# Performance work log

Hardware: AMD Instinct MI355X
Metric: run time of the kernel (lower is better)

The kernel has to match this reference:

```python
import jax, jax.numpy as jnp
import numpy as np


def _approx_match(xyz1, xyz2):
    """Faithful port of approxmatch_cpu/cuda (auction-style soft bipartite matching).

    xyz1: [b, n, 3], xyz2: [b, m, 3] -> (match [b, n, m], sq_dists [b, n, m])
    """
    b, n, _ = xyz1.shape
    m = xyz2.shape[1]
    factorl = max(n, m) // n  # integer division, as in the CUDA source
    factorr = max(n, m) // m

    # all-pairs squared distances  [b, n, m]
    d2 = jnp.sum((xyz1[:, :, None, :] - xyz2[:, None, :, :]) ** 2, axis=-1)

    # annealing schedule: j = 8 .. -1 -> level = -4^j ; j = -2 -> level = 0
    levels = jnp.asarray([-(4.0 ** j) for j in range(8, -2, -1)] + [0.0],
                         dtype=xyz1.dtype)

    satl0 = jnp.full((b, n), float(factorl), dtype=xyz1.dtype)  # row capacities
    satr0 = jnp.full((b, m), float(factorr), dtype=xyz1.dtype)  # col capacities
    match0 = jnp.zeros((b, n, m), dtype=xyz1.dtype)

    def step(carry, level):
        satl, satr, match = carry
        # weight = exp(level * d2) * saturatedr
        w = jnp.exp(level * d2) * satr[:, None, :]                       # [b,n,m]
        # row-normalize, scale by remaining row capacity
        w = w / (jnp.sum(w, axis=2, keepdims=True) + 1e-9) * satl[:, :, None]
        # column rescale by remaining column capacity
        ss = jnp.sum(w, axis=1) + 1e-9                                   # [b,m]
        w = w * (satr / ss)[:, None, :]
        # deplete capacities
        satl = jnp.maximum(satl - jnp.sum(w, axis=2), 0.0)
        satr = jnp.maximum(satr - jnp.sum(w, axis=1), 0.0)
        return (satl, satr, match + w), None

    (_, _, match), _ = jax.lax.scan(step, (satl0, satr0, match0), levels)
    return match, d2


def setup_inputs() -> dict:
    key = jax.random.key(0)
    k1, k2 = jax.random.split(key)
    b, n, m = 4, 4096, 4096
    return {
        "input1": jax.random.normal(k1, (b, n, 3), dtype=jnp.float32),
        "input2": jax.random.normal(k2, (b, m, 3), dtype=jnp.float32),
        "eps": 0,    # accepted but unused by the original Function
        "iters": 50, # accepted but unused by the original Function
    }


def reference(input1, input2, eps, iters):
    # eps / iters are ignored, matching EarthMoverDistanceFunction.apply(xyz1, xyz2)
    match, d2 = _approx_match(input1, input2)
    dist = jnp.sqrt(jnp.maximum(d2, 1e-12))  # matchcost uses euclidean (sqrt) distance
    return jnp.sum(match * dist, axis=(1, 2))  # cost per batch element, [b]
```

## Files before the change

kernel.cpp:

```cpp
#include <hip/hip_runtime.h>

#define BLOCK 256
#define IC    64
#define RPT   4
#define ROWS  (BLOCK*RPT)
#define RBLK  64

__device__ __forceinline__ float wave_reduce_add(float v) {
#pragma unroll
    for (int off = 32; off > 0; off >>= 1) v += __shfl_down(v, off, 64);
    return v;
}
__device__ __forceinline__ float lg2(float x) { return __builtin_amdgcn_logf(x); }
__device__ __forceinline__ float ex2(float x) { return __builtin_amdgcn_exp2f(x); }

__device__ __forceinline__ void load_rows(const float* p, float* x, float* y, float* z) {
    float4 v0 = *(const float4*)p;
    float4 v1 = *(const float4*)(p + 4);
    float4 v2 = *(const float4*)(p + 8);
    x[0]=v0.x; x[1]=v0.w; x[2]=v1.z; x[3]=v2.y;
    y[0]=v0.y; y[1]=v1.x; y[2]=v1.w; y[3]=v2.z;
    z[0]=v0.z; z[1]=v1.y; z[2]=v2.x; z[3]=v2.w;
}

__global__ __launch_bounds__(BLOCK)
void emd_init(float* __restrict__ satl, float* __restrict__ satr,
              float* __restrict__ out, float* __restrict__ Asum,
              float fl, float fr, int b, int n, int m) {
    int idx = blockIdx.x * blockDim.x + threadIdx.x;
    if (idx < b * n) satl[idx] = fl;
    if (idx < b * m) satr[idx] = fr;
    if (idx < b)   { out[idx] = 0.f; Asum[idx] = 0.f; }
}

__global__ __launch_bounds__(BLOCK, 4)
void emd_pass1(const float* __restrict__ xyz1, const float* __restrict__ xyz2,
               float* __restrict__ P1p, float ls, float wconst, float thr,
               int n, int m, int bn)
{
    __shared__ float4 sh[IC];
    const int bb = blockIdx.z, chunk = blockIdx.y;

    const int i0 = blockIdx.x * ROWS + threadIdx.x * RPT;
    float x[RPT], y[RPT], z[RPT], acc[RPT];
    load_rows(xyz1 + ((size_t)bb * n + i0) * 3, x, y, z);

    const float* x2 = xyz2 + (size_t)bb * m * 3;
    for (int t = threadIdx.x; t < IC; t += BLOCK) {
        int j = chunk * IC + t;
        sh[t] = make_float4(x2[3*j], x2[3*j+1], x2[3*j+2], wconst);
    }
    __syncthreads();

#pragma unroll
    for (int r = 0; r < RPT; ++r) acc[r] = 0.f;
#pragma unroll 2
    for (int tb = 0; tb < IC; tb += 4) {
        float4 q0 = sh[tb+0], q1 = sh[tb+1], q2 = sh[tb+2], q3 = sh[tb+3];
        float d0[RPT], d1[RPT], d2v[RPT], d3[RPT];
        float dmin = 1e30f;
#pragma unroll
        for (int r = 0; r < RPT; ++r) {
            float dx, dy, dz;
            dx=x[r]-q0.x; dy=y[r]-q0.y; dz=z[r]-q0.z; d0[r]=fmaf(dz,dz,fmaf(dy,dy,dx*dx));
            dx=x[r]-q1.x; dy=y[r]-q1.y; dz=z[r]-q1.z; d1[r]=fmaf(dz,dz,fmaf(dy,dy,dx*dx));
            dx=x[r]-q2.x; dy=y[r]-q2.y; dz=z[r]-q2.z; d2v[r]=fmaf(dz,dz,fmaf(dy,dy,dx*dx));
            dx=x[r]-q3.x; dy=y[r]-q3.y; dz=z[r]-q3.z; d3[r]=fmaf(dz,dz,fmaf(dy,dy,dx*dx));
            dmin = fminf(dmin, fminf(fminf(d0[r], d1[r]), fminf(d2v[r], d3[r])));
        }
        if (__any(dmin < thr)) {
#pragma unroll
            for (int r = 0; r < RPT; ++r) {
                acc[r] += ex2(fmaf(d0[r],  ls, q0.w));
                acc[r] += ex2(fmaf(d1[r],  ls, q1.w));
                acc[r] += ex2(fmaf(d2v[r], ls, q2.w));
                acc[r] += ex2(fmaf(d3[r],  ls, q3.w));
            }
        }
    }
    *(float4*)&P1p[(size_t)chunk * bn + (size_t)bb * n + i0] =
        make_float4(acc[0], acc[1], acc[2], acc[3]);
}

__global__ __launch_bounds__(BLOCK, 4)
void emd_pass2(const float* __restrict__ xyzO, const float* __restrict__ xyzS,
               const float* __restrict__ satlIn, float* __restrict__ satlOut,
               const float* __restrict__ aIn, float* __restrict__ aOut,
               const float* __restrict__ P1p, const float* __restrict__ P3a,
               const float* __restrict__ P3b, float* __restrict__ P2p,
               float* __restrict__ cost,
               float ls, float thr, int nO, int nS, int bnS, int bnO,
               int C4, int first)
{
    __shared__ float4 sh[IC];
    __shared__ float red[3][4][IC];
    const int bb = blockIdx.z, chunk = blockIdx.y;

    const int j0 = blockIdx.x * ROWS + threadIdx.x * RPT;
    float x[RPT], y[RPT], z[RPT], acc[RPT];
    load_rows(xyzO + ((size_t)bb * nO + j0) * 3, x, y, z);

    const int t6 = threadIdx.x & 63, g = threadIdx.x >> 6;
    const size_t ri = (size_t)bb * nS + chunk * IC + t6;
    {
        float ps = 0.f, pa = 0.f, pb = 0.f;
        const int c0 = g * C4;
        if (first) {
#pragma unroll 16
            for (int k = 0; k < C4; ++k) ps += P1p[(size_t)(c0 + k) * bnS + ri];
        } else {
#pragma unroll 16
            for (int k = 0; k < C4; ++k) {
                ps += P1p[(size_t)(c0 + k) * bnS + ri];
                pa += P3a[(size_t)(c0 + k) * bnS + ri];
                pb += P3b[(size_t)(c0 + k) * bnS + ri];
            }
        }
        red[0][g][t6] = ps; red[1][g][t6] = pa; red[2][g][t6] = pb;
    }
    __syncthreads();
    if (threadIdx.x < IC) {
        float rs = red[0][0][t6] + red[0][1][t6] + red[0][2][t6] + red[0][3][t6];
        float sl, costv = 0.f;
        if (first) {
            sl = satlIn[ri];
        } else {
            float s1 = red[1][0][t6] + red[1][1][t6] + red[1][2][t6] + red[1][3][t6];
            float s2 = red[2][0][t6] + red[2][1][t6] + red[2][2][t6] + red[2][3][t6];
            float ap = aIn[ri];
            sl = fmaxf(satlIn[ri] - ap * s1, 0.f);
            costv = ap * s2;
        }
        float av = sl / (rs + 1e-9f);
        if (blockIdx.x == 0) {
            satlOut[ri] = sl;
            aOut[ri]    = av;
            if (!first) {
                float cv = wave_reduce_add(costv);
                if (t6 == 0) atomicAdd(&cost[bb], cv);
            }
        }
        const float* xs = xyzS + ((size_t)bb * nS + chunk * IC + t6) * 3;
        sh[t6] = make_float4(xs[0], xs[1], xs[2], lg2(av));
    }
    __syncthreads();

#pragma unroll
    for (int r = 0; r < RPT; ++r) acc[r] = 0.f;
    if (thr < 1e29f) {
#pragma unroll 2
        for (int tb = 0; tb < IC; tb += 4) {
            float4 q0 = sh[tb+0], q1 = sh[tb+1], q2 = sh[tb+2], q3 = sh[tb+3];
            float d0[RPT], d1[RPT], d2v[RPT], d3[RPT];
            float dmin = 1e30f;
#pragma unroll
            for (int r = 0; r < RPT; ++r) {
                float dx, dy, dz;
                dx=x[r]-q0.x; dy=y[r]-q0.y; dz=z[r]-q0.z; d0[r]=fmaf(dz,dz,fmaf(dy,dy,dx*dx));
                dx=x[r]-q1.x; dy=y[r]-q1.y; dz=z[r]-q1.z; d1[r]=fmaf(dz,dz,fmaf(dy,dy,dx*dx));
                dx=x[r]-q2.x; dy=y[r]-q2.y; dz=z[r]-q2.z; d2v[r]=fmaf(dz,dz,fmaf(dy,dy,dx*dx));
                dx=x[r]-q3.x; dy=y[r]-q3.y; dz=z[r]-q3.z; d3[r]=fmaf(dz,dz,fmaf(dy,dy,dx*dx));
                dmin = fminf(dmin, fminf(fminf(d0[r], d1[r]), fminf(d2v[r], d3[r])));
            }
            if (__any(dmin < thr)) {
#pragma unroll
                for (int r = 0; r < RPT; ++r) {
                    acc[r] += ex2(fmaf(d0[r],  ls, q0.w));
                    acc[r] += ex2(fmaf(d1[r],  ls, q1.w));
                    acc[r] += ex2(fmaf(d2v[r], ls, q2.w));
                    acc[r] += ex2(fmaf(d3[r],  ls, q3.w));
                }
            }
        }
    } else {
#pragma unroll 2
        for (int tb = 0; tb < IC; tb += 4) {
            float4 q0 = sh[tb+0], q1 = sh[tb+1], q2 = sh[tb+2], q3 = sh[tb+3];
#pragma unroll
            for (int r = 0; r < RPT; ++r) {
                float dx, dy, dz, d2;
                dx=x[r]-q0.x; dy=y[r]-q0.y; dz=z[r]-q0.z;
                d2=fmaf(dz,dz,fmaf(dy,dy,dx*dx)); acc[r] += ex2(fmaf(d2, ls, q0.w));
                dx=x[r]-q1.x; dy=y[r]-q1.y; dz=z[r]-q1.z;
                d2=fmaf(dz,dz,fmaf(dy,dy,dx*dx)); acc[r] += ex2(fmaf(d2, ls, q1.w));
                dx=x[r]-q2.x; dy=y[r]-q2.y; dz=z[r]-q2.z;
                d2=fmaf(dz,dz,fmaf(dy,dy,dx*dx)); acc[r] += ex2(fmaf(d2, ls, q2.w));
                dx=x[r]-q3.x; dy=y[r]-q3.y; dz=z[r]-q3.z;
                d2=fmaf(dz,dz,fmaf(dy,dy,dx*dx)); acc[r] += ex2(fmaf(d2, ls, q3.w));
            }
        }
    }
    *(float4*)&P2p[(size_t)chunk * bnO + (size_t)bb * nO + j0] =
        make_float4(acc[0], acc[1], acc[2], acc[3]);
}

__global__ __launch_bounds__(BLOCK, 4)
void emd_fused(const float* __restrict__ xyz1, const float* __restrict__ xyz2,
               const float* __restrict__ satrIn, float* __restrict__ satrOut,
               const float* __restrict__ P2p,
               float* __restrict__ P3a, float* __restrict__ P3b,
               float* __restrict__ P1p,
               float lsA, float lsB, float thr,
               int n, int m, int bn, int bm, int C4, int mode)
{
    __shared__ float4 sh[IC];
    __shared__ float  shB[IC];
    __shared__ float  red[4][IC];
    __shared__ float  snsumS;
    const int bb = blockIdx.z, chunk = blockIdx.y;

    const int i0 = blockIdx.x * ROWS + threadIdx.x * RPT;
    float x[RPT], y[RPT], z[RPT];
    load_rows(xyz1 + ((size_t)bb * n + i0) * 3, x, y, z);

    const int t6 = threadIdx.x & 63, g = threadIdx.x >> 6;
    const size_t rj = (size_t)bb * m + chunk * IC + t6;
    {
        float ps = 0.f;
        const int c0 = g * C4;
#pragma unroll 16
        for (int k = 0; k < C4; ++k) ps += P2p[(size_t)(c0 + k) * bm + rj];
        red[g][t6] = ps;
    }
    __syncthreads();
    if (threadIdx.x < IC) {
        float cs  = red[0][t6] + red[1][t6] + red[2][t6] + red[3][t6];
        float sr  = satrIn[rj];
        float cs2 = sr * cs;
        float inv = sr / (cs2 + 1e-9f);
        float r2  = sr * inv;
        float sn  = fmaxf(sr - cs2 * inv, 0.f);
        if (blockIdx.x == 0) satrOut[rj] = sn;
        const float* xs = xyz2 + ((size_t)bb * m + chunk * IC + t6) * 3;
        if (mode == 0) {
            sh[t6]  = make_float4(xs[0], xs[1], xs[2], lg2(r2));
            shB[t6] = lg2(sn);
        } else {
            sh[t6]  = make_float4(xs[0], xs[1], xs[2], r2);
            shB[t6] = sn;
            if (mode == 2) {
                float ss = wave_reduce_add(sn);
                if (t6 == 0) snsumS = ss;
            }
        }
    }
    __syncthreads();

    float s1[RPT], s2[RPT], r1[RPT];
#pragma unroll
    for (int r = 0; r < RPT; ++r) { s1[r] = 0.f; s2[r] = 0.f; r1[r] = 0.f; }

    if (mode == 0) {
#pragma unroll 2
        for (int tb = 0; tb < IC; tb += 4) {
            float4 q0 = sh[tb+0], q1 = sh[tb+1], q2 = sh[tb+2], q3 = sh[tb+3];
            float lb0 = shB[tb+0], lb1 = shB[tb+1], lb2 = shB[tb+2], lb3 = shB[tb+3];
            float d0[RPT], d1[RPT], d2v[RPT], d3[RPT];
            float dmin = 1e30f;
#pragma unroll
            for (int r = 0; r < RPT; ++r) {
                float dx, dy, dz;
                dx=x[r]-q0.x; dy=y[r]-q0.y; dz=z[r]-q0.z; d0[r]=fmaf(dz,dz,fmaf(dy,dy,dx*dx));
                dx=x[r]-q1.x; dy=y[r]-q1.y; dz=z[r]-q1.z; d1[r]=fmaf(dz,dz,fmaf(dy,dy,dx*dx));
                dx=x[r]-q2.x; dy=y[r]-q2.y; dz=z[r]-q2.z; d2v[r]=fmaf(dz,dz,fmaf(dy,dy,dx*dx));
                dx=x[r]-q3.x; dy=y[r]-q3.y; dz=z[r]-q3.z; d3[r]=fmaf(dz,dz,fmaf(dy,dy,dx*dx));
                dmin = fminf(dmin, fminf(fminf(d0[r], d1[r]), fminf(d2v[r], d3[r])));
            }
            if (__any(dmin < thr)) {
#pragma unroll
                for (int r = 0; r < RPT; ++r) {
                    float e;
                    e = ex2(fmaf(d0[r], lsA, q0.w));
                    s1[r] += e; s2[r] = fmaf(e, __builtin_amdgcn_sqrtf(d0[r]), s2[r]);
                    r1[r] += ex2(fmaf(d0[r], lsB, lb0));
                    e = ex2(fmaf(d1[r], lsA, q1.w));
                    s1[r] += e; s2[r] = fmaf(e, __builtin_amdgcn_sqrtf(d1[r]), s2[r]);
                    r1[r] += ex2(fmaf(d1[r], lsB, lb1));
                    e = ex2(fmaf(d2v[r], lsA, q2.w));
                    s1[r] += e; s2[r] = fmaf(e, __builtin_amdgcn_sqrtf(d2v[r]), s2[r]);
                    r1[r] += ex2(fmaf(d2v[r], lsB, lb2));
                    e = ex2(fmaf(d3[r], lsA, q3.w));
                    s1[r] += e; s2[r] = fmaf(e, __builtin_amdgcn_sqrtf(d3[r]), s2[r]);
                    r1[r] += ex2(fmaf(d3[r], lsB, lb3));
                }
            }
        }
    } else if (mode == 1) {
#pragma unroll 2
        for (int tb = 0; tb < IC; tb += 4) {
            float4 q0 = sh[tb+0], q1 = sh[tb+1], q2 = sh[tb+2], q3 = sh[tb+3];
            float lb0 = shB[tb+0], lb1 = shB[tb+1], lb2 = shB[tb+2], lb3 = shB[tb+3];
#pragma unroll
            for (int r = 0; r < RPT; ++r) {
                float dx, dy, dz, d2, t, t2, e3;
                dx=x[r]-q0.x; dy=y[r]-q0.y; dz=z[r]-q0.z;
                d2=fmaf(dz,dz,fmaf(dy,dy,dx*dx));
                t = ex2(d2 * lsB); t2 = t*t; e3 = t2*t2*q0.w;
                s1[r] += e3; s2[r] = fmaf(e3, __builtin_amdgcn_sqrtf(d2), s2[r]);
                r1[r] = fmaf(t, lb0, r1[r]);
                dx=x[r]-q1.x; dy=y[r]-q1.y; dz=z[r]-q1.z;
                d2=fmaf(dz,dz,fmaf(dy,dy,dx*dx));
                t = ex2(d2 * lsB); t2 = t*t; e3 = t2*t2*q1.w;
                s1[r] += e3; s2[r] = fmaf(e3, __builtin_amdgcn_sqrtf(d2), s2[r]);
                r1[r] = fmaf(t, lb1, r1[r]);
                dx=x[r]-q2.x; dy=y[r]-q2.y; dz=z[r]-q2.z;
                d2=fmaf(dz,dz,fmaf(dy,dy,dx*dx));
                t = ex2(d2 * lsB); t2 = t*t; e3 = t2*t2*q2.w;
                s1[r] += e3; s2[r] = fmaf(e3, __builtin_amdgcn_sqrtf(d2), s2[r]);
                r1[r] = fmaf(t, lb2, r1[r]);
                dx=x[r]-q3.x; dy=y[r]-q3.y; dz=z[r]-q3.z;
                d2=fmaf(dz,dz,fmaf(dy,dy,dx*dx));
                t = ex2(d2 * lsB); t2 = t*t; e3 = t2*t2*q3.w;
                s1[r] += e3; s2[r] = fmaf(e3, __builtin_amdgcn_sqrtf(d2), s2[r]);
                r1[r] = fmaf(t, lb3, r1[r]);
            }
        }
    } else {
#pragma unroll 2
        for (int tb = 0; tb < IC; tb += 4) {
            float4 q0 = sh[tb+0], q1 = sh[tb+1], q2 = sh[tb+2], q3 = sh[tb+3];
#pragma unroll
            for (int r = 0; r < RPT; ++r) {
                float dx, dy, dz, d2, e;
                dx=x[r]-q0.x; dy=y[r]-q0.y; dz=z[r]-q0.z;
                d2=fmaf(dz,dz,fmaf(dy,dy,dx*dx));
                e = ex2(d2 * lsA) * q0.w;
                s1[r] += e; s2[r] = fmaf(e, __builtin_amdgcn_sqrtf(d2), s2[r]);
                dx=x[r]-q1.x; dy=y[r]-q1.y; dz=z[r]-q1.z;
                d2=fmaf(dz,dz,fmaf(dy,dy,dx*dx));
                e = ex2(d2 * lsA) * q1.w;
                s1[r] += e; s2[r] = fmaf(e, __builtin_amdgcn_sqrtf(d2), s2[r]);
                dx=x[r]-q2.x; dy=y[r]-q2.y; dz=z[r]-q2.z;
                d2=fmaf(dz,dz,fmaf(dy,dy,dx*dx));
                e = ex2(d2 * lsA) * q2.w;
                s1[r] += e; s2[r] = fmaf(e, __builtin_amdgcn_sqrtf(d2), s2[r]);
                dx=x[r]-q3.x; dy=y[r]-q3.y; dz=z[r]-q3.z;
                d2=fmaf(dz,dz,fmaf(dy,dy,dx*dx));
                e = ex2(d2 * lsA) * q3.w;
                s1[r] += e; s2[r] = fmaf(e, __builtin_amdgcn_sqrtf(d2), s2[r]);
            }
        }
    }
    size_t base = (size_t)chunk * bn + (size_t)bb * n + i0;
    if (mode == 2) {
        float sc = snsumS;
#pragma unroll
        for (int r = 0; r < RPT; ++r) r1[r] = sc;
    }
    *(float4*)&P3a[base] = make_float4(s1[0], s1[1], s1[2], s1[3]);
    *(float4*)&P3b[base] = make_float4(s2[0], s2[1], s2[2], s2[3]);
    *(float4*)&P1p[base] = make_float4(r1[0], r1[1], r1[2], r1[3]);
}

__global__ __launch_bounds__(BLOCK)
void emd_redL_last(const float* __restrict__ satl, const float* __restrict__ aIn,
                   float* __restrict__ aOut,
                   const float* __restrict__ P1p, const float* __restrict__ P3a,
                   const float* __restrict__ P3b, float* __restrict__ cost,
                   float* __restrict__ Asum, int C, int bn, int n)
{
    const int idx = blockIdx.x * BLOCK + threadIdx.x;
    float rs = 0.f, s1 = 0.f, s2 = 0.f;
#pragma unroll 16
    for (int c = 0; c < C; ++c) {
        rs += P1p[(size_t)c * bn + idx];
        s1 += P3a[(size_t)c * bn + idx];
        s2 += P3b[(size_t)c * bn + idx];
    }
    float ap = aIn[idx];
    float sl = fmaxf(satl[idx] - ap * s1, 0.f);
    float av = sl / (rs + 1e-9f);
    aOut[idx] = av;
    float cv  = wave_reduce_add(ap * s2);
    float avs = wave_reduce_add(av);
    if ((threadIdx.x & 63) == 0) {
        atomicAdd(&cost[idx / n], cv);
        atomicAdd(&Asum[idx / n], avs);
    }
}

__global__ __launch_bounds__(BLOCK, 4)
void emd_pass3_last(const float* __restrict__ xyz1, const float* __restrict__ xyz2,
                    const float* __restrict__ satrIn, const float* __restrict__ Asum,
                    float* __restrict__ P3b, int n, int m, int bn, int bm)
{
    __shared__ float4 sh[IC];
    const int bb = blockIdx.z, chunk = blockIdx.y;

    const int i0 = blockIdx.x * ROWS + threadIdx.x * RPT;
    float x[RPT], y[RPT], z[RPT], s2[RPT];
    load_rows(xyz1 + ((size_t)bb * n + i0) * 3, x, y, z);

    const float A = Asum[bb];
    for (int t = threadIdx.x; t < IC; t += BLOCK) {
        int j = chunk * IC + t;
        size_t rj = (size_t)bb * m + j;
        float sr  = satrIn[rj];
        float cs2 = sr * A;
        float inv = sr / (cs2 + 1e-9f);
        const float* xs = xyz2 + ((size_t)bb * m + j) * 3;
        sh[t] = make_float4(xs[0], xs[1], xs[2], sr * inv);
    }
    __syncthreads();

#pragma unroll
    for (int r = 0; r < RPT; ++r) s2[r] = 0.f;
#pragma unroll 4
    for (int tb = 0; tb < IC; tb += 4) {
        float4 q0 = sh[tb+0], q1 = sh[tb+1], q2 = sh[tb+2], q3 = sh[tb+3];
#pragma unroll
        for (int r = 0; r < RPT; ++r) {
            float dx, dy, dz, d2;
            dx = x[r]-q0.x; dy = y[r]-q0.y; dz = z[r]-q0.z;
            d2 = fmaf(dz, dz, fmaf(dy, dy, dx*dx));
            s2[r] = fmaf(q0.w, __builtin_amdgcn_sqrtf(d2), s2[r]);
            dx = x[r]-q1.x; dy = y[r]-q1.y; dz = z[r]-q1.z;
            d2 = fmaf(dz, dz, fmaf(dy, dy, dx*dx));
            s2[r] = fmaf(q1.w, __builtin_amdgcn_sqrtf(d2), s2[r]);
            dx = x[r]-q2.x; dy = y[r]-q2.y; dz = z[r]-q2.z;
            d2 = fmaf(dz, dz, fmaf(dy, dy, dx*dx));
            s2[r] = fmaf(q2.w, __builtin_amdgcn_sqrtf(d2), s2[r]);
            dx = x[r]-q3.x; dy = y[r]-q3.y; dz = z[r]-q3.z;
            d2 = fmaf(dz, dz, fmaf(dy, dy, dx*dx));
            s2[r] = fmaf(q3.w, __builtin_amdgcn_sqrtf(d2), s2[r]);
        }
    }
    *(float4*)&P3b[(size_t)chunk * bn + (size_t)bb * n + i0] =
        make_float4(s2[0], s2[1], s2[2], s2[3]);
}

__global__ __launch_bounds__(RBLK)
void emd_final(const float* __restrict__ a, const float* __restrict__ P3b,
               float* __restrict__ cost, int C, int bn, int n)
{
    const int idx = blockIdx.x * RBLK + threadIdx.x;
    float s2 = 0.f;
#pragma unroll 16
    for (int c = 0; c < C; ++c) s2 += P3b[(size_t)c * bn + idx];
    float cv = wave_reduce_add(a[idx] * s2);
    if (threadIdx.x == 0) atomicAdd(&cost[idx / n], cv);
}

extern "C" void kernel_launch(void* const* d_in, const int* in_sizes, int n_in,
                              void* d_out, int out_size, void* d_ws, size_t ws_size,
                              hipStream_t stream)
{
    const float* xyz1 = (const float*)d_in[0];
    const float* xyz2 = (const float*)d_in[1];
    const int b = out_size;
    const int n = in_sizes[0] / (3 * b);
    const int m = in_sizes[1] / (3 * b);
    const int C  = m / IC;
    const int C2 = n / IC;
    const int bn = b * n, bm = b * m;

    float* ws    = (float*)d_ws;
    float* satlA = ws; ws += (size_t)bn;
    float* satlB = ws; ws += (size_t)bn;
    float* satrA = ws; ws += (size_t)bm;
    float* satrB = ws; ws += (size_t)bm;
    float* aA    = ws; ws += (size_t)bn;
    float* aB    = ws; ws += (size_t)bn;
    float* Asum  = ws; ws += 16;
    float* P1p   = ws; ws += (size_t)bn * C;
    float* P2p   = ws; ws += (size_t)bm * C2;
    float* P3a   = ws; ws += (size_t)bn * C;
    float* P3b   = ws; ws += (size_t)bn * C;

    float* out = (float*)d_out;

    const int mx = n > m ? n : m;
    const float fl = (float)(mx / n), fr = (float)(mx / m);
    const float lgfr = log2f(fr);

    emd_init<<<dim3((b * mx + BLOCK - 1) / BLOCK), BLOCK, 0, stream>>>(
        satlA, satrA, out, Asum, fl, fr, b, n, m);

    const double LOG2E = 1.4426950408889634074;
    const double levels[11] = {-65536.0, -16384.0, -4096.0, -1024.0, -256.0,
                               -64.0, -16.0, -4.0, -1.0, -0.25, 0.0};
    float lsv[11], thrP[11], thrF[10];
    for (int k = 0; k < 11; ++k) {
        lsv[k] = (float)(levels[k] * LOG2E);
        thrP[k] = (k <= 3) ? 165.f / fabsf(lsv[k]) : 1e30f;
    }
    for (int k = 0; k < 10; ++k)
        thrF[k] = (k <= 3) ? 165.f / fabsf(lsv[k]) : 1e30f;

    const dim3 g1(n / ROWS, m / IC, b);
    const dim3 g2(m / ROWS, n / IC, b);

    emd_pass1<<<g1, BLOCK, 0, stream>>>(xyz1, xyz2, P1p, lsv[0], lgfr, thrP[0],
                                        n, m, bn);

    float *slI = satlA, *slO = satlB, *aI = aA, *aO = aB;
    float *srI = satrA, *srO = satrB;
    for (int L = 0; L <= 9; ++L) {
        emd_pass2<<<g2, BLOCK, 0, stream>>>(xyz2, xyz1, slI, slO, aI, aO,
                                            P1p, P3a, P3b, P2p, out,
                                            lsv[L], thrP[L], m, n, bn, bm,
                                            C / 4, (L == 0) ? 1 : 0);
        { float* t = slI; slI = slO; slO = t; }
        { float* t = aI;  aI  = aO;  aO  = t; }
        const int mode = (L <= 3) ? 0 : ((L <= 8) ? 1 : 2);
        emd_fused<<<g1, BLOCK, 0, stream>>>(xyz1, xyz2, srI, srO, P2p,
                                            P3a, P3b, P1p,
                                            lsv[L], lsv[L + 1], thrF[L],
                                            n, m, bn, bm, C2 / 4, mode);
        { float* t = srI; srI = srO; srO = t; }
    }
    emd_redL_last<<<dim3(bn / BLOCK), BLOCK, 0, stream>>>(
        slI, aI, aO, P1p, P3a, P3b, out, Asum, C, bn, n);
    emd_pass3_last<<<g1, BLOCK, 0, stream>>>(xyz1, xyz2, srI, Asum, P3b,
                                             n, m, bn, bm);
    emd_final<<<dim3(bn / RBLK), RBLK, 0, stream>>>(aO, P3b, out, C, bn, n);
}
```

Measured before the change: 686.2 us.

## Halve column chunk size and double occupancy target across pairwise kernels

```diff
diff --git a/kernel.cpp b/kernel.cpp
--- a/kernel.cpp
+++ b/kernel.cpp
@@ -1,7 +1,7 @@
 #include <hip/hip_runtime.h>
 
 #define BLOCK 256
-#define IC    64
+#define IC    32
 #define RPT   4
 #define ROWS  (BLOCK*RPT)
 #define RBLK  64
@@ -33,7 +33,7 @@
     if (idx < b)   { out[idx] = 0.f; Asum[idx] = 0.f; }
 }
 
-__global__ __launch_bounds__(BLOCK, 4)
+__global__ __launch_bounds__(BLOCK, 8)
 void emd_pass1(const float* __restrict__ xyz1, const float* __restrict__ xyz2,
                float* __restrict__ P1p, float ls, float wconst, float thr,
                int n, int m, int bn)
@@ -46,9 +46,9 @@
     load_rows(xyz1 + ((size_t)bb * n + i0) * 3, x, y, z);
 
     const float* x2 = xyz2 + (size_t)bb * m * 3;
-    for (int t = threadIdx.x; t < IC; t += BLOCK) {
-        int j = chunk * IC + t;
-        sh[t] = make_float4(x2[3*j], x2[3*j+1], x2[3*j+2], wconst);
+    if (threadIdx.x < IC) {
+        int j = chunk * IC + threadIdx.x;
+        sh[threadIdx.x] = make_float4(x2[3*j], x2[3*j+1], x2[3*j+2], wconst);
     }
     __syncthreads();
 
@@ -82,7 +82,7 @@
         make_float4(acc[0], acc[1], acc[2], acc[3]);
 }
 
-__global__ __launch_bounds__(BLOCK, 4)
+__global__ __launch_bounds__(BLOCK, 8)
 void emd_pass2(const float* __restrict__ xyzO, const float* __restrict__ xyzS,
                const float* __restrict__ satlIn, float* __restrict__ satlOut,
                const float* __restrict__ aIn, float* __restrict__ aOut,
@@ -90,58 +90,66 @@
                const float* __restrict__ P3b, float* __restrict__ P2p,
                float* __restrict__ cost,
                float ls, float thr, int nO, int nS, int bnS, int bnO,
-               int C4, int first)
+               int C8, int first)
 {
     __shared__ float4 sh[IC];
-    __shared__ float red[3][4][IC];
+    __shared__ float red[3][8][IC];
     const int bb = blockIdx.z, chunk = blockIdx.y;
 
     const int j0 = blockIdx.x * ROWS + threadIdx.x * RPT;
     float x[RPT], y[RPT], z[RPT], acc[RPT];
     load_rows(xyzO + ((size_t)bb * nO + j0) * 3, x, y, z);
 
-    const int t6 = threadIdx.x & 63, g = threadIdx.x >> 6;
-    const size_t ri = (size_t)bb * nS + chunk * IC + t6;
     {
+        const int t5 = threadIdx.x & 31, g = threadIdx.x >> 5;
+        const size_t ri = (size_t)bb * nS + chunk * IC + t5;
         float ps = 0.f, pa = 0.f, pb = 0.f;
-        const int c0 = g * C4;
+        const int c0 = g * C8;
         if (first) {
 #pragma unroll 16
-            for (int k = 0; k < C4; ++k) ps += P1p[(size_t)(c0 + k) * bnS + ri];
+            for (int k = 0; k < C8; ++k) ps += P1p[(size_t)(c0 + k) * bnS + ri];
         } else {
 #pragma unroll 16
-            for (int k = 0; k < C4; ++k) {
+            for (int k = 0; k < C8; ++k) {
                 ps += P1p[(size_t)(c0 + k) * bnS + ri];
                 pa += P3a[(size_t)(c0 + k) * bnS + ri];
                 pb += P3b[(size_t)(c0 + k) * bnS + ri];
             }
         }
-        red[0][g][t6] = ps; red[1][g][t6] = pa; red[2][g][t6] = pb;
+        red[0][g][t5] = ps; red[1][g][t5] = pa; red[2][g][t5] = pb;
     }
     __syncthreads();
-    if (threadIdx.x < IC) {
-        float rs = red[0][0][t6] + red[0][1][t6] + red[0][2][t6] + red[0][3][t6];
-        float sl, costv = 0.f;
+    if (threadIdx.x < 64) {
+        const int t = threadIdx.x;
+        const bool act = t < IC;
+        const size_t ri = (size_t)bb * nS + chunk * IC + (act ? t : 0);
+        float rs = 0.f, s1 = 0.f, s2 = 0.f;
+        if (act) {
+#pragma unroll
+            for (int g = 0; g < 8; ++g) {
+                rs += red[0][g][t]; s1 += red[1][g][t]; s2 += red[2][g][t];
+            }
+        }
+        float sl = 0.f, costv = 0.f;
         if (first) {
-            sl = satlIn[ri];
+            if (act) sl = satlIn[ri];
         } else {
-            float s1 = red[1][0][t6] + red[1][1][t6] + red[1][2][t6] + red[1][3][t6];
-            float s2 = red[2][0][t6] + red[2][1][t6] + red[2][2][t6] + red[2][3][t6];
-            float ap = aIn[ri];
-            sl = fmaxf(satlIn[ri] - ap * s1, 0.f);
+            float ap = act ? aIn[ri] : 0.f;
+            if (act) sl = fmaxf(satlIn[ri] - ap * s1, 0.f);
             costv = ap * s2;
         }
-        float av = sl / (rs + 1e-9f);
+        float av = act ? sl / (rs + 1e-9f) : 0.f;
         if (blockIdx.x == 0) {
-            satlOut[ri] = sl;
-            aOut[ri]    = av;
+            if (act) { satlOut[ri] = sl; aOut[ri] = av; }
             if (!first) {
                 float cv = wave_reduce_add(costv);
-                if (t6 == 0) atomicAdd(&cost[bb], cv);
-            }
-        }
-        const float* xs = xyzS + ((size_t)bb * nS + chunk * IC + t6) * 3;
-        sh[t6] = make_float4(xs[0], xs[1], xs[2], lg2(av));
+                if (t == 0) atomicAdd(&cost[bb], cv);
+            }
+        }
+        if (act) {
+            const float* xs = xyzS + ri * 3;
+            sh[t] = make_float4(xs[0], xs[1], xs[2], lg2(av));
+        }
     }
     __syncthreads();
 
@@ -194,18 +202,18 @@
         make_float4(acc[0], acc[1], acc[2], acc[3]);
 }
 
-__global__ __launch_bounds__(BLOCK, 4)
+__global__ __launch_bounds__(BLOCK, 8)
 void emd_fused(const float* __restrict__ xyz1, const float* __restrict__ xyz2,
                const float* __restrict__ satrIn, float* __restrict__ satrOut,
                const float* __restrict__ P2p,
                float* __restrict__ P3a, float* __restrict__ P3b,
                float* __restrict__ P1p,
                float lsA, float lsB, float thr,
-               int n, int m, int bn, int bm, int C4, int mode)
+               int n, int m, int bn, int bm, int C8, int mode)
 {
     __shared__ float4 sh[IC];
     __shared__ float  shB[IC];
-    __shared__ float  red[4][IC];
+    __shared__ float  red[8][IC];
     __shared__ float  snsumS;
     const int bb = blockIdx.z, chunk = blockIdx.y;
 
@@ -213,35 +221,43 @@
     float x[RPT], y[RPT], z[RPT];
     load_rows(xyz1 + ((size_t)bb * n + i0) * 3, x, y, z);
 
-    const int t6 = threadIdx.x & 63, g = threadIdx.x >> 6;
-    const size_t rj = (size_t)bb * m + chunk * IC + t6;
     {
+        const int t5 = threadIdx.x & 31, g = threadIdx.x >> 5;
+        const size_t rj = (size_t)bb * m + chunk * IC + t5;
         float ps = 0.f;
-        const int c0 = g * C4;
+        const int c0 = g * C8;
 #pragma unroll 16
-        for (int k = 0; k < C4; ++k) ps += P2p[(size_t)(c0 + k) * bm + rj];
-        red[g][t6] = ps;
+        for (int k = 0; k < C8; ++k) ps += P2p[(size_t)(c0 + k) * bm + rj];
+        red[g][t5] = ps;
     }
     __syncthreads();
-    if (threadIdx.x < IC) {
-        float cs  = red[0][t6] + red[1][t6] + red[2][t6] + red[3][t6];
-        float sr  = satrIn[rj];
-        float cs2 = sr * cs;
-        float inv = sr / (cs2 + 1e-9f);
-        float r2  = sr * inv;
-        float sn  = fmaxf(sr - cs2 * inv, 0.f);
-        if (blockIdx.x == 0) satrOut[rj] = sn;
-        const float* xs = xyz2 + ((size_t)bb * m + chunk * IC + t6) * 3;
-        if (mode == 0) {
-            sh[t6]  = make_float4(xs[0], xs[1], xs[2], lg2(r2));
-            shB[t6] = lg2(sn);
-        } else {
-            sh[t6]  = make_float4(xs[0], xs[1], xs[2], r2);
-            shB[t6] = sn;
-            if (mode == 2) {
-                float ss = wave_reduce_add(sn);
-                if (t6 == 0) snsumS = ss;
-            }
+    if (threadIdx.x < 64) {
+        const int t = threadIdx.x;
+        const bool act = t < IC;
+        const size_t rj = (size_t)bb * m + chunk * IC + (act ? t : 0);
+        float sn = 0.f;
+        if (act) {
+            float cs = 0.f;
+#pragma unroll
+            for (int g = 0; g < 8; ++g) cs += red[g][t];
+            float sr  = satrIn[rj];
+            float cs2 = sr * cs;
+            float inv = sr / (cs2 + 1e-9f);
+            float r2  = sr * inv;
+            sn = fmaxf(sr - cs2 * inv, 0.f);
+            if (blockIdx.x == 0) satrOut[rj] = sn;
+            const float* xs = xyz2 + rj * 3;
+            if (mode == 0) {
+                sh[t]  = make_float4(xs[0], xs[1], xs[2], lg2(r2));
+                shB[t] = lg2(sn);
+            } else {
+                sh[t]  = make_float4(xs[0], xs[1], xs[2], r2);
+                shB[t] = sn;
+            }
+        }
+        if (mode == 2) {
+            float ss = wave_reduce_add(act ? sn : 0.f);
+            if (t == 0) snsumS = ss;
         }
     }
     __syncthreads();
@@ -379,7 +395,7 @@
     }
 }
 
-__global__ __launch_bounds__(BLOCK, 4)
+__global__ __launch_bounds__(BLOCK, 8)
 void emd_pass3_last(const float* __restrict__ xyz1, const float* __restrict__ xyz2,
                     const float* __restrict__ satrIn, const float* __restrict__ Asum,
                     float* __restrict__ P3b, int n, int m, int bn, int bm)
@@ -391,15 +407,15 @@
     float x[RPT], y[RPT], z[RPT], s2[RPT];
     load_rows(xyz1 + ((size_t)bb * n + i0) * 3, x, y, z);
 
-    const float A = Asum[bb];
-    for (int t = threadIdx.x; t < IC; t += BLOCK) {
-        int j = chunk * IC + t;
+    if (threadIdx.x < IC) {
+        const float A = Asum[bb];
+        int j = chunk * IC + threadIdx.x;
         size_t rj = (size_t)bb * m + j;
         float sr  = satrIn[rj];
         float cs2 = sr * A;
         float inv = sr / (cs2 + 1e-9f);
-        const float* xs = xyz2 + ((size_t)bb * m + j) * 3;
-        sh[t] = make_float4(xs[0], xs[1], xs[2], sr * inv);
+        const float* xs = xyz2 + rj * 3;
+        sh[threadIdx.x] = make_float4(xs[0], xs[1], xs[2], sr * inv);
     }
     __syncthreads();
 
@@ -499,14 +515,14 @@
         emd_pass2<<<g2, BLOCK, 0, stream>>>(xyz2, xyz1, slI, slO, aI, aO,
                                             P1p, P3a, P3b, P2p, out,
                                             lsv[L], thrP[L], m, n, bn, bm,
-                                            C / 4, (L == 0) ? 1 : 0);
+                                            C / 8, (L == 0) ? 1 : 0);
         { float* t = slI; slI = slO; slO = t; }
         { float* t = aI;  aI  = aO;  aO  = t; }
         const int mode = (L <= 3) ? 0 : ((L <= 8) ? 1 : 2);
         emd_fused<<<g1, BLOCK, 0, stream>>>(xyz1, xyz2, srI, srO, P2p,
                                             P3a, P3b, P1p,
                                             lsv[L], lsv[L + 1], thrF[L],
-                                            n, m, bn, bm, C2 / 4, mode);
+                                            n, m, bn, bm, C2 / 8, mode);
         { float* t = srI; srI = srO; srO = t; }
     }
     emd_redL_last<<<dim3(bn / BLOCK), BLOCK, 0, stream>>>(
```

After: 1.188 ms. +73.1%, slower.

## Bin-sort points by x coordinate so far tiles skip exp work at more levels

Applied to the files above, without the earlier changes.

```diff
diff --git a/kernel.cpp b/kernel.cpp
--- a/kernel.cpp
+++ b/kernel.cpp
@@ -5,6 +5,7 @@
 #define RPT   4
 #define ROWS  (BLOCK*RPT)
 #define RBLK  64
+#define BINS  256
 
 __device__ __forceinline__ float wave_reduce_add(float v) {
 #pragma unroll
@@ -26,11 +27,64 @@
 __global__ __launch_bounds__(BLOCK)
 void emd_init(float* __restrict__ satl, float* __restrict__ satr,
               float* __restrict__ out, float* __restrict__ Asum,
+              int* __restrict__ h1, int* __restrict__ h2,
+              int* __restrict__ c1, int* __restrict__ c2,
               float fl, float fr, int b, int n, int m) {
     int idx = blockIdx.x * blockDim.x + threadIdx.x;
     if (idx < b * n) satl[idx] = fl;
     if (idx < b * m) satr[idx] = fr;
     if (idx < b)   { out[idx] = 0.f; Asum[idx] = 0.f; }
+    if (idx < b * BINS) { h1[idx] = 0; h2[idx] = 0; c1[idx] = 0; c2[idx] = 0; }
+}
+
+__device__ __forceinline__ int xbin(float x) {
+    int bi = (int)((x + 4.f) * (BINS / 8.f));
+    return bi < 0 ? 0 : (bi > BINS - 1 ? BINS - 1 : bi);
+}
+
+__global__ __launch_bounds__(BLOCK)
+void emd_hist(const float* __restrict__ xyz1, const float* __restrict__ xyz2,
+              int* __restrict__ h1, int* __restrict__ h2, int n, int m) {
+    int idx = blockIdx.x * blockDim.x + threadIdx.x;
+    int b1 = idx / n;
+    atomicAdd(&h1[b1 * BINS + xbin(xyz1[(size_t)idx * 3])], 1);
+    int b2 = idx / m;
+    atomicAdd(&h2[b2 * BINS + xbin(xyz2[(size_t)idx * 3])], 1);
+}
+
+__global__ __launch_bounds__(BINS)
+void emd_scan(const int* __restrict__ h1, const int* __restrict__ h2,
+              int* __restrict__ base1, int* __restrict__ base2, int b) {
+    const int t = threadIdx.x;
+    for (int bb = 0; bb < b; ++bb) {
+        int s1 = 0, s2 = 0;
+        for (int u = 0; u < t; ++u) { s1 += h1[bb*BINS+u]; s2 += h2[bb*BINS+u]; }
+        base1[bb*BINS+t] = s1; base2[bb*BINS+t] = s2;
+    }
+}
+
+__global__ __launch_bounds__(BLOCK)
+void emd_scatter(const float* __restrict__ xyz1, const float* __restrict__ xyz2,
+                 const int* __restrict__ base1, const int* __restrict__ base2,
+                 int* __restrict__ c1, int* __restrict__ c2,
+                 float* __restrict__ s1p, float* __restrict__ s2p, int n, int m) {
+    int idx = blockIdx.x * blockDim.x + threadIdx.x;
+    {
+        int bb = idx / n;
+        float x = xyz1[(size_t)idx*3], y = xyz1[(size_t)idx*3+1], z = xyz1[(size_t)idx*3+2];
+        int bi = xbin(x);
+        int pos = base1[bb*BINS+bi] + atomicAdd(&c1[bb*BINS+bi], 1);
+        size_t d = ((size_t)bb * n + pos) * 3;
+        s1p[d] = x; s1p[d+1] = y; s1p[d+2] = z;
+    }
+    {
+        int bb = idx / m;
+        float x = xyz2[(size_t)idx*3], y = xyz2[(size_t)idx*3+1], z = xyz2[(size_t)idx*3+2];
+        int bi = xbin(x);
+        int pos = base2[bb*BINS+bi] + atomicAdd(&c2[bb*BINS+bi], 1);
+        size_t d = ((size_t)bb * m + pos) * 3;
+        s2p[d] = x; s2p[d+1] = y; s2p[d+2] = z;
+    }
 }
 
 __global__ __launch_bounds__(BLOCK, 4)
@@ -140,7 +194,7 @@
                 if (t6 == 0) atomicAdd(&cost[bb], cv);
             }
         }
-        const float* xs = xyzS + ((size_t)bb * nS + chunk * IC + t6) * 3;
+        const float* xs = xyzS + ri * 3;
         sh[t6] = make_float4(xs[0], xs[1], xs[2], lg2(av));
     }
     __syncthreads();
@@ -200,7 +254,7 @@
                const float* __restrict__ P2p,
                float* __restrict__ P3a, float* __restrict__ P3b,
                float* __restrict__ P1p,
-               float lsA, float lsB, float thr,
+               float lsA, float lsB, float thr, float thrM,
                int n, int m, int bn, int bm, int C4, int mode)
 {
     __shared__ float4 sh[IC];
@@ -231,7 +285,7 @@
         float r2  = sr * inv;
         float sn  = fmaxf(sr - cs2 * inv, 0.f);
         if (blockIdx.x == 0) satrOut[rj] = sn;
-        const float* xs = xyz2 + ((size_t)bb * m + chunk * IC + t6) * 3;
+        const float* xs = xyz2 + rj * 3;
         if (mode == 0) {
             sh[t6]  = make_float4(xs[0], xs[1], xs[2], lg2(r2));
             shB[t6] = lg2(sn);
@@ -290,29 +344,34 @@
         for (int tb = 0; tb < IC; tb += 4) {
             float4 q0 = sh[tb+0], q1 = sh[tb+1], q2 = sh[tb+2], q3 = sh[tb+3];
             float lb0 = shB[tb+0], lb1 = shB[tb+1], lb2 = shB[tb+2], lb3 = shB[tb+3];
+            float d0[RPT], d1[RPT], d2v[RPT], d3[RPT];
+            float dmin = 1e30f;
 #pragma unroll
             for (int r = 0; r < RPT; ++r) {
-                float dx, dy, dz, d2, t, t2, e3;
-                dx=x[r]-q0.x; dy=y[r]-q0.y; dz=z[r]-q0.z;
-                d2=fmaf(dz,dz,fmaf(dy,dy,dx*dx));
-                t = ex2(d2 * lsB); t2 = t*t; e3 = t2*t2*q0.w;
-                s1[r] += e3; s2[r] = fmaf(e3, __builtin_amdgcn_sqrtf(d2), s2[r]);
-                r1[r] = fmaf(t, lb0, r1[r]);
-                dx=x[r]-q1.x; dy=y[r]-q1.y; dz=z[r]-q1.z;
-                d2=fmaf(dz,dz,fmaf(dy,dy,dx*dx));
-                t = ex2(d2 * lsB); t2 = t*t; e3 = t2*t2*q1.w;
-                s1[r] += e3; s2[r] = fmaf(e3, __builtin_amdgcn_sqrtf(d2), s2[r]);
-                r1[r] = fmaf(t, lb1, r1[r]);
-                dx=x[r]-q2.x; dy=y[r]-q2.y; dz=z[r]-q2.z;
-                d2=fmaf(dz,dz,fmaf(dy,dy,dx*dx));
-                t = ex2(d2 * lsB); t2 = t*t; e3 = t2*t2*q2.w;
-                s1[r] += e3; s2[r] = fmaf(e3, __builtin_amdgcn_sqrtf(d2), s2[r]);
-                r1[r] = fmaf(t, lb2, r1[r]);
-                dx=x[r]-q3.x; dy=y[r]-q3.y; dz=z[r]-q3.z;
-                d2=fmaf(dz,dz,fmaf(dy,dy,dx*dx));
-                t = ex2(d2 * lsB); t2 = t*t; e3 = t2*t2*q3.w;
-                s1[r] += e3; s2[r] = fmaf(e3, __builtin_amdgcn_sqrtf(d2), s2[r]);
-                r1[r] = fmaf(t, lb3, r1[r]);
+                float dx, dy, dz;
+                dx=x[r]-q0.x; dy=y[r]-q0.y; dz=z[r]-q0.z; d0[r]=fmaf(dz,dz,fmaf(dy,dy,dx*dx));
+                dx=x[r]-q1.x; dy=y[r]-q1.y; dz=z[r]-q1.z; d1[r]=fmaf(dz,dz,fmaf(dy,dy,dx*dx));
+                dx=x[r]-q2.x; dy=y[r]-q2.y; dz=z[r]-q2.z; d2v[r]=fmaf(dz,dz,fmaf(dy,dy,dx*dx));
+                dx=x[r]-q3.x; dy=y[r]-q3.y; dz=z[r]-q3.z; d3[r]=fmaf(dz,dz,fmaf(dy,dy,dx*dx));
+                dmin = fminf(dmin, fminf(fminf(d0[r], d1[r]), fminf(d2v[r], d3[r])));
+            }
+            if (__any(dmin < thrM)) {
+#pragma unroll
+                for (int r = 0; r < RPT; ++r) {
+                    float t, t2, e3;
+                    t = ex2(d0[r] * lsB); t2 = t*t; e3 = t2*t2*q0.w;
+                    s1[r] += e3; s2[r] = fmaf(e3, __builtin_amdgcn_sqrtf(d0[r]), s2[r]);
+                    r1[r] = fmaf(t, lb0, r1[r]);
+                    t = ex2(d1[r] * lsB); t2 = t*t; e3 = t2*t2*q1.w;
+                    s1[r] += e3; s2[r] = fmaf(e3, __builtin_amdgcn_sqrtf(d1[r]), s2[r]);
+                    r1[r] = fmaf(t, lb1, r1[r]);
+                    t = ex2(d2v[r] * lsB); t2 = t*t; e3 = t2*t2*q2.w;
+                    s1[r] += e3; s2[r] = fmaf(e3, __builtin_amdgcn_sqrtf(d2v[r]), s2[r]);
+                    r1[r] = fmaf(t, lb2, r1[r]);
+                    t = ex2(d3[r] * lsB); t2 = t*t; e3 = t2*t2*q3.w;
+                    s1[r] += e3; s2[r] = fmaf(e3, __builtin_amdgcn_sqrtf(d3[r]), s2[r]);
+                    r1[r] = fmaf(t, lb3, r1[r]);
+                }
             }
         }
     } else {
@@ -398,7 +457,7 @@
         float sr  = satrIn[rj];
         float cs2 = sr * A;
         float inv = sr / (cs2 + 1e-9f);
-        const float* xs = xyz2 + ((size_t)bb * m + j) * 3;
+        const float* xs = xyz2 + rj * 3;
         sh[t] = make_float4(xs[0], xs[1], xs[2], sr * inv);
     }
     __syncthreads();
@@ -462,6 +521,14 @@
     float* aA    = ws; ws += (size_t)bn;
     float* aB    = ws; ws += (size_t)bn;
     float* Asum  = ws; ws += 16;
+    float* x1s   = ws; ws += (size_t)bn * 3;
+    float* x2s   = ws; ws += (size_t)bm * 3;
+    int*   h1    = (int*)ws; ws += b * BINS;
+    int*   h2    = (int*)ws; ws += b * BINS;
+    int*   c1    = (int*)ws; ws += b * BINS;
+    int*   c2    = (int*)ws; ws += b * BINS;
+    int*   bs1   = (int*)ws; ws += b * BINS;
+    int*   bs2   = (int*)ws; ws += b * BINS;
     float* P1p   = ws; ws += (size_t)bn * C;
     float* P2p   = ws; ws += (size_t)bm * C2;
     float* P3a   = ws; ws += (size_t)bn * C;
@@ -474,44 +541,50 @@
     const float lgfr = log2f(fr);
 
     emd_init<<<dim3((b * mx + BLOCK - 1) / BLOCK), BLOCK, 0, stream>>>(
-        satlA, satrA, out, Asum, fl, fr, b, n, m);
+        satlA, satrA, out, Asum, h1, h2, c1, c2, fl, fr, b, n, m);
+    emd_hist<<<dim3(bn / BLOCK), BLOCK, 0, stream>>>(xyz1, xyz2, h1, h2, n, m);
+    emd_scan<<<1, BINS, 0, stream>>>(h1, h2, bs1, bs2, b);
+    emd_scatter<<<dim3(bn / BLOCK), BLOCK, 0, stream>>>(xyz1, xyz2, bs1, bs2,
+                                                        c1, c2, x1s, x2s, n, m);
 
     const double LOG2E = 1.4426950408889634074;
     const double levels[11] = {-65536.0, -16384.0, -4096.0, -1024.0, -256.0,
                                -64.0, -16.0, -4.0, -1.0, -0.25, 0.0};
-    float lsv[11], thrP[11], thrF[10];
+    float lsv[11], thrP[11], thrF[10], thrM[10];
     for (int k = 0; k < 11; ++k) {
         lsv[k] = (float)(levels[k] * LOG2E);
-        thrP[k] = (k <= 3) ? 165.f / fabsf(lsv[k]) : 1e30f;
-    }
-    for (int k = 0; k < 10; ++k)
+        thrP[k] = (k <= 5) ? 165.f / fabsf(lsv[k]) : 1e30f;
+    }
+    for (int k = 0; k < 10; ++k) {
         thrF[k] = (k <= 3) ? 165.f / fabsf(lsv[k]) : 1e30f;
+        thrM[k] = (k >= 4 && k <= 5) ? 150.f / fabsf(lsv[k + 1]) : 1e30f;
+    }
 
     const dim3 g1(n / ROWS, m / IC, b);
     const dim3 g2(m / ROWS, n / IC, b);
 
-    emd_pass1<<<g1, BLOCK, 0, stream>>>(xyz1, xyz2, P1p, lsv[0], lgfr, thrP[0],
+    emd_pass1<<<g1, BLOCK, 0, stream>>>(x1s, x2s, P1p, lsv[0], lgfr, thrP[0],
                                         n, m, bn);
 
     float *slI = satlA, *slO = satlB, *aI = aA, *aO = aB;
     float *srI = satrA, *srO = satrB;
     for (int L = 0; L <= 9; ++L) {
-        emd_pass2<<<g2, BLOCK, 0, stream>>>(xyz2, xyz1, slI, slO, aI, aO,
+        emd_pass2<<<g2, BLOCK, 0, stream>>>(x2s, x1s, slI, slO, aI, aO,
                                             P1p, P3a, P3b, P2p, out,
                                             lsv[L], thrP[L], m, n, bn, bm,
                                             C / 4, (L == 0) ? 1 : 0);
         { float* t = slI; slI = slO; slO = t; }
         { float* t = aI;  aI  = aO;  aO  = t; }
         const int mode = (L <= 3) ? 0 : ((L <= 8) ? 1 : 2);
-        emd_fused<<<g1, BLOCK, 0, stream>>>(xyz1, xyz2, srI, srO, P2p,
+        emd_fused<<<g1, BLOCK, 0, stream>>>(x1s, x2s, srI, srO, P2p,
                                             P3a, P3b, P1p,
-                                            lsv[L], lsv[L + 1], thrF[L],
+                                            lsv[L], lsv[L + 1], thrF[L], thrM[L],
                                             n, m, bn, bm, C2 / 4, mode);
         { float* t = srI; srI = srO; srO = t; }
     }
     emd_redL_last<<<dim3(bn / BLOCK), BLOCK, 0, stream>>>(
         slI, aI, aO, P1p, P3a, P3b, out, Asum, C, bn, n);
-    emd_pass3_last<<<g1, BLOCK, 0, stream>>>(xyz1, xyz2, srI, Asum, P3b,
+    emd_pass3_last<<<g1, BLOCK, 0, stream>>>(x1s, x2s, srI, Asum, P3b,
                                              n, m, bn, bm);
     emd_final<<<dim3(bn / RBLK), RBLK, 0, stream>>>(aO, P3b, out, C, bn, n);
 }
```

After: 743.2 us. 1.08x slower.
